# Optimization experiments

Hardware: AMD Instinct MI355X
Metric: run time of the kernel (lower is better)

## Reference

```python
import jax, jax.numpy as jnp
import numpy as np


def setup_inputs() -> dict:
    key = jax.random.key(0)
    ks = jax.random.split(key, 9)
    B, T, C = 4, 2048, 2048
    E, I, SI = 8, 1408, 5632
    s = lambda k, shape, fan_in: jax.random.normal(k, shape, jnp.float32) * (fan_in ** -0.5)
    return {
        "x": jax.random.normal(ks[0], (B, T, C), jnp.float32),
        "gate_w": s(ks[1], (C, E), C),                  # router: x @ gate_w -> [N,E]
        "expert_gate_w": s(ks[2], (E, C, I), C),        # stacked gate_proj weights
        "expert_up_w": s(ks[3], (E, C, I), C),          # stacked up_proj weights
        "expert_down_w": s(ks[4], (E, I, C), I),        # stacked down_proj weights
        "shared_gate_w": s(ks[5], (C, SI), C),
        "shared_up_w": s(ks[6], (C, SI), C),
        "shared_down_w": s(ks[7], (SI, C), SI),
        "shared_expert_gate_w": s(ks[8], (C, 1), C),
        "top_k": 4,
    }


def reference(x, gate_w, expert_gate_w, expert_up_w, expert_down_w,
              shared_gate_w, shared_up_w, shared_down_w, shared_expert_gate_w, top_k):
    B, T, C = x.shape
    E = gate_w.shape[1]
    xf = x.reshape(-1, C)                      # [N, C]
    N = xf.shape[0]

    # --- router: softmax (fp32) -> top-k -> renormalize ---
    logits = xf @ gate_w                       # [N, E]
    probs = jax.nn.softmax(logits.astype(jnp.float32), axis=-1)
    w, idx = jax.lax.top_k(probs, top_k)       # [N, k]
    w = w / jnp.sum(w, axis=-1, keepdims=True)

    # dense combine gates [N, E]: zero for non-selected experts (equivalent to
    # the torch dispatch/sort/combine: each token gets weight w_k on expert idx_k)
    gates = jnp.zeros((N, E), jnp.float32).at[jnp.arange(N)[:, None], idx].add(w)

    # --- per-expert SwiGLU MLP, accumulated via scan over experts ---
    def step(acc, ew):
        wg, wu, wd, g = ew                     # wg/wu: [C,I], wd: [I,C], g: [N]
        h = jax.nn.silu(xf @ wg) * (xf @ wu)   # [N, I]
        return acc + g[:, None] * (h @ wd), None

    routed, _ = jax.lax.scan(
        step, jnp.zeros_like(xf),
        (expert_gate_w, expert_up_w, expert_down_w, gates.T))

    # --- shared expert with sigmoid gate ---
    shared = (jax.nn.silu(xf @ shared_gate_w) * (xf @ shared_up_w)) @ shared_down_w
    sg = jax.nn.sigmoid(xf @ shared_expert_gate_w)   # [N, 1]

    return (routed + sg * shared).reshape(B, T, C)
```

## Files before the change

### kernel.cpp

```cpp
#include <hip/hip_runtime.h>
#include <hip/hip_bf16.h>
#include <stdint.h>


typedef float f32x4 __attribute__((ext_vector_type(4)));
typedef int   i32x4 __attribute__((ext_vector_type(4)));
typedef __hip_bfloat16 bf16;

#define DEV __device__ __forceinline__

DEV void mfma16(f32x4& c, const i32x4& a, const i32x4& b) {
    asm("v_mfma_f32_16x16x32_bf16 %0, %1, %2, %0" : "+v"(c) : "v"(a), "v"(b));
}

template<int ROWS>
DEV void stage(const bf16* gtile, long ldK, char* lds, int tid) {
    const int wid = tid >> 6, lane = tid & 63;
    const int swz = ((lane & 7) ^ (lane >> 3)) << 4;
    constexpr int NISS = (ROWS * 128) / 4096;
    #pragma unroll
    for (int i = 0; i < NISS; i++) {
        const int o = i * 4096 + wid * 1024;
        const int row = (o >> 7) + (lane >> 3);
        const char* ga = (const char*)gtile + (long)row * (ldK * 2) + swz;
        __builtin_amdgcn_global_load_lds(
            (const __attribute__((address_space(1))) void*)ga,
            (__attribute__((address_space(3))) void*)(lds + o), 16, 0, 0);
    }
}

template<int ROWS>
DEV void stage_idx(const char* base, const long* roff, int ktb, char* lds,
                   int tid, int swz) {
    const int wid = tid >> 6;
    constexpr int NISS = (ROWS * 128) / 4096;
    #pragma unroll
    for (int i = 0; i < NISS; i++) {
        const int o = i * 4096 + wid * 1024;
        const char* ga = base + roff[i] + ktb + swz;
        __builtin_amdgcn_global_load_lds(
            (const __attribute__((address_space(1))) void*)ga,
            (__attribute__((address_space(3))) void*)(lds + o), 16, 0, 0);
    }
}

DEV i32x4 ldsfrag(const char* lds, int row, int kbyte) {
    const int off = (row << 7) + (kbyte ^ ((row & 7) << 4));
    return *(const i32x4*)(lds + off);
}

__global__ __launch_bounds__(256) void tcvt(const float* __restrict__ src,
        bf16* __restrict__ dst, int Cd, long dld) {
    __shared__ float t[64][65];
    const int cb = blockIdx.x * 64, rb = blockIdx.y * 64;
    const int tx = threadIdx.x & 63, ty = threadIdx.x >> 6;
    #pragma unroll
    for (int i = 0; i < 16; i++) {
        const int r = ty + i * 4;
        t[r][tx] = src[(long)(rb + r) * Cd + cb + tx];
    }
    __syncthreads();
    #pragma unroll
    for (int i = 0; i < 16; i++) {
        const int c = ty + i * 4;
        dst[(long)(cb + c) * dld + rb + tx] = __float2bfloat16(t[tx][c]);
    }
}

__global__ __launch_bounds__(256) void cvtx(const float* __restrict__ x,
        bf16* __restrict__ xb, long n4) {
    long i = (long)blockIdx.x * blockDim.x + threadIdx.x;
    const long stride = (long)gridDim.x * blockDim.x;
    for (; i < n4; i += stride) {
        const float4 v = ((const float4*)x)[i];
        union { bf16 h[4]; ushort4 u; } cu;
        cu.h[0] = __float2bfloat16(v.x); cu.h[1] = __float2bfloat16(v.y);
        cu.h[2] = __float2bfloat16(v.z); cu.h[3] = __float2bfloat16(v.w);
        ((ushort4*)xb)[i] = cu.u;
    }
}

__global__ __launch_bounds__(256) void router(const float* __restrict__ x,
        const float* __restrict__ gw, const float* __restrict__ segw,
        int* __restrict__ tidx, float* __restrict__ tw,
        float* __restrict__ sg, int C) {
    const int lane = threadIdx.x & 63;
    const long t = (long)blockIdx.x * 4 + (threadIdx.x >> 6);
    const float* xr = x + t * C;
    float a[9];
    #pragma unroll
    for (int e = 0; e < 9; e++) a[e] = 0.f;
    for (int c = lane; c < C; c += 64) {
        const float xv = xr[c];
        const float4* g4 = (const float4*)(gw + (long)c * 8);
        const float4 g0 = g4[0], g1 = g4[1];
        a[0] += xv * g0.x; a[1] += xv * g0.y; a[2] += xv * g0.z; a[3] += xv * g0.w;
        a[4] += xv * g1.x; a[5] += xv * g1.y; a[6] += xv * g1.z; a[7] += xv * g1.w;
        a[8] += xv * segw[c];
    }
    #pragma unroll
    for (int e = 0; e < 9; e++) {
        #pragma unroll
        for (int o = 32; o; o >>= 1) a[e] += __shfl_xor(a[e], o, 64);
    }
    if (lane == 0) {
        float m = a[0];
        #pragma unroll
        for (int e = 1; e < 8; e++) m = fmaxf(m, a[e]);
        float p[8]; float s = 0.f;
        #pragma unroll
        for (int e = 0; e < 8; e++) { p[e] = expf(a[e] - m); s += p[e]; }
        #pragma unroll
        for (int e = 0; e < 8; e++) p[e] /= s;
        bool used[8] = {false,false,false,false,false,false,false,false};
        float wsum = 0.f; int idx[4]; float wv[4];
        for (int k = 0; k < 4; k++) {
            float best = -1.f; int bi = 0;
            for (int e = 0; e < 8; e++)
                if (!used[e] && p[e] > best) { best = p[e]; bi = e; }
            used[bi] = true; idx[k] = bi; wv[k] = best; wsum += best;
        }
        int4 iv; float4 wv4;
        iv.x = idx[0]; iv.y = idx[1]; iv.z = idx[2]; iv.w = idx[3];
        wv4.x = wv[0] / wsum; wv4.y = wv[1] / wsum;
        wv4.z = wv[2] / wsum; wv4.w = wv[3] / wsum;
        ((int4*)tidx)[t] = iv;
        ((float4*)tw)[t] = wv4;
        sg[t] = 1.f / (1.f + expf(-a[8]));
    }
}

__global__ __launch_bounds__(256) void build_lists(const int* __restrict__ tidx,
        const float* __restrict__ tw, int* __restrict__ tok,
        float* __restrict__ wl, int* __restrict__ cnt, int N) {
    const int e = blockIdx.x;
    const int tid = threadIdx.x;
    const int per = N / 256;
    __shared__ int csum[256];
    int c = 0;
    for (int i = 0; i < per; i++) {
        const int4 id4 = ((const int4*)tidx)[tid * per + i];
        if (id4.x == e || id4.y == e || id4.z == e || id4.w == e) c++;
    }
    csum[tid] = c;
    __syncthreads();
    for (int o = 1; o < 256; o <<= 1) {
        const int v = (tid >= o) ? csum[tid - o] : 0;
        __syncthreads();
        csum[tid] += v;
        __syncthreads();
    }
    int pos = csum[tid] - c;
    if (tid == 255) cnt[e] = csum[255];
    for (int i = 0; i < per; i++) {
        const int t = tid * per + i;
        const int4   id4 = ((const int4*)tidx)[t];
        const float4 w4  = ((const float4*)tw)[t];
        float w = 0.f; int hit = 0;
        if      (id4.x == e) { w = w4.x; hit = 1; }
        else if (id4.y == e) { w = w4.y; hit = 1; }
        else if (id4.z == e) { w = w4.z; hit = 1; }
        else if (id4.w == e) { w = w4.w; hit = 1; }
        if (hit) { tok[(long)e * N + pos] = t; wl[(long)e * N + pos] = w; pos++; }
    }
}

__global__ __launch_bounds__(256) void dual_gemm(const bf16* __restrict__ A,
        const int* __restrict__ ridx, const int* __restrict__ cntp, int Mfix,
        const bf16* __restrict__ BG, const bf16* __restrict__ BU,
        bf16* __restrict__ H, long hld,
        const float* __restrict__ sc, int K) {
    __shared__ __align__(128) char Al[16384];
    __shared__ __align__(128) char Gl[8192];
    __shared__ __align__(128) char Ul[8192];
    const int Me = cntp ? *cntp : Mfix;
    const long m0 = (long)blockIdx.x * 128;
    if (m0 >= Me) return;
    const int tid = threadIdx.x, lane = tid & 63, wid = tid >> 6;
    const long n0 = (long)blockIdx.y * 64;
    const int wm = (wid >> 1) * 64, wn = (wid & 1) * 32;
    const int l15 = lane & 15, lhi = lane >> 4;
    const int swz = ((lane & 7) ^ (lane >> 3)) << 4;
    long roffA[4];
    #pragma unroll
    for (int i = 0; i < 4; i++) {
        const int rit = ((i * 4096 + wid * 1024) >> 7) + (lane >> 3);
        int g = (int)m0 + rit;
        if (ridx) g = ridx[g < Me ? g : Me - 1];
        roffA[i] = (long)g * (K * 2);
    }
    f32x4 ag[4][2] = {}; f32x4 au[4][2] = {};
    for (int kt = 0; kt < K; kt += 64) {
        stage_idx<128>((const char*)A, roffA, kt * 2, Al, tid, swz);
        stage<64>(BG + n0 * K + kt, (long)K, Gl, tid);
        stage<64>(BU + n0 * K + kt, (long)K, Ul, tid);
        __syncthreads();
        #pragma unroll
        for (int ks = 0; ks < 2; ks++) {
            const int kb = ks * 64 + lhi * 16;
            i32x4 af[4], bg[2], bu[2];
            #pragma unroll
            for (int mi = 0; mi < 4; mi++) af[mi] = ldsfrag(Al, wm + mi * 16 + l15, kb);
            #pragma unroll
            for (int ni = 0; ni < 2; ni++) {
                bg[ni] = ldsfrag(Gl, wn + ni * 16 + l15, kb);
                bu[ni] = ldsfrag(Ul, wn + ni * 16 + l15, kb);
            }
            #pragma unroll
            for (int mi = 0; mi < 4; mi++) {
                #pragma unroll
                for (int ni = 0; ni < 2; ni++) {
                    mfma16(ag[mi][ni], af[mi], bg[ni]);
                    mfma16(au[mi][ni], af[mi], bu[ni]);
                }
            }
        }
        __syncthreads();
    }
    asm volatile("s_nop 7\n\ts_nop 7\n\ts_nop 7");
    #pragma unroll
    for (int mi = 0; mi < 4; mi++) {
        #pragma unroll
        for (int r = 0; r < 4; r++) {
            const int pos = (int)m0 + wm + mi * 16 + lhi * 4 + r;
            if (pos < Me) {
                const float s = sc[pos];
                #pragma unroll
                for (int ni = 0; ni < 2; ni++) {
                    const float gv = ag[mi][ni][r], uv = au[mi][ni][r];
                    const float h = (gv / (1.f + expf(-gv))) * uv * s;
                    H[(long)pos * hld + n0 + wn + ni * 16 + l15] = __float2bfloat16(h);
                }
            }
        }
    }
}

__global__ __launch_bounds__(256) void gemm_down(const bf16* __restrict__ A,
        const bf16* __restrict__ BT, float* __restrict__ C,
        const int* __restrict__ ridx, const int* __restrict__ cntp, int Mfix,
        int K, long ldc, int beta) {
    __shared__ __align__(128) char Al[16384];
    __shared__ __align__(128) char Bl[16384];
    const int Me = cntp ? *cntp : Mfix;
    const long m0 = (long)blockIdx.y * 128;
    if (m0 >= Me) return;
    const int tid = threadIdx.x, lane = tid & 63, wid = tid >> 6;
    const long n0 = (long)blockIdx.x * 128;
    const int wm = (wid >> 1) * 64, wn = (wid & 1) * 64;
    const int l15 = lane & 15, lhi = lane >> 4;
    f32x4 acc[4][4] = {};
    for (int kt = 0; kt < K; kt += 64) {
        stage<128>(A  + m0 * K + kt, (long)K, Al, tid);
        stage<128>(BT + n0 * K + kt, (long)K, Bl, tid);
        __syncthreads();
        #pragma unroll
        for (int ks = 0; ks < 2; ks++) {
            const int kb = ks * 64 + lhi * 16;
            i32x4 af[4], bfr[4];
            #pragma unroll
            for (int mi = 0; mi < 4; mi++) af[mi]  = ldsfrag(Al, wm + mi * 16 + l15, kb);
            #pragma unroll
            for (int ni = 0; ni < 4; ni++) bfr[ni] = ldsfrag(Bl, wn + ni * 16 + l15, kb);
            #pragma unroll
            for (int mi = 0; mi < 4; mi++) {
                #pragma unroll
                for (int ni = 0; ni < 4; ni++) mfma16(acc[mi][ni], af[mi], bfr[ni]);
            }
        }
        __syncthreads();
    }
    asm volatile("s_nop 7\n\ts_nop 7\n\ts_nop 7");
    #pragma unroll
    for (int mi = 0; mi < 4; mi++) {
        #pragma unroll
        for (int r = 0; r < 4; r++) {
            const int pos = (int)m0 + wm + mi * 16 + lhi * 4 + r;
            if (pos < Me) {
                const long orow = ridx ? (long)ridx[pos] : (long)pos;
                #pragma unroll
                for (int ni = 0; ni < 4; ni++) {
                    const long ci = orow * ldc + n0 + wn + ni * 16 + l15;
                    float v = acc[mi][ni][r];
                    if (beta) v += C[ci];
                    C[ci] = v;
                }
            }
        }
    }
}

extern "C" void kernel_launch(void* const* d_in, const int* in_sizes, int n_in,
                              void* d_out, int out_size, void* d_ws, size_t ws_size,
                              hipStream_t stream) {
    const int N = 8192, Cdim = 2048, E = 8, I = 1408, SI = 5632;

    const float* x    = (const float*)d_in[0];
    const float* gw   = (const float*)d_in[1];
    const float* egw  = (const float*)d_in[2];
    const float* euw  = (const float*)d_in[3];
    const float* edw  = (const float*)d_in[4];
    const float* sgw  = (const float*)d_in[5];
    const float* suw  = (const float*)d_in[6];
    const float* sdw  = (const float*)d_in[7];
    const float* segw = (const float*)d_in[8];
    float* out = (float*)d_out;

    char* ws = (char*)d_ws;
    size_t off = 0;
    auto alloc = [&](size_t bytes) { char* p = ws + off; off += (bytes + 255) & ~(size_t)255; return p; };

    bf16*  xb   = (bf16*) alloc((size_t)N * Cdim * 2);
    int*   tidx = (int*)  alloc((size_t)N * 4 * 4);
    float* tw   = (float*)alloc((size_t)N * 4 * 4);
    float* sg   = (float*)alloc((size_t)N * 4);
    int*   tok  = (int*)  alloc((size_t)E * N * 4);
    float* wl   = (float*)alloc((size_t)E * N * 4);
    int*   cnt  = (int*)  alloc(256);
    const size_t commonEnd = off;

    bf16* Wu   = (bf16*)alloc((size_t)I * Cdim * 2);
    bf16* WgWd = (bf16*)alloc((size_t)I * Cdim * 2);
    bf16* Hc   = (bf16*)alloc((size_t)N * I * 2);
    if (off > ws_size) return;

    cvtx<<<4096, 256, 0, stream>>>(x, xb, (long)N * Cdim / 4);
    router<<<N / 4, 256, 0, stream>>>(x, gw, segw, tidx, tw, sg, Cdim);
    build_lists<<<E, 256, 0, stream>>>(tidx, tw, tok, wl, cnt, N);

    const size_t bigSharedNeed = commonEnd
        + 2 * (size_t)SI * Cdim * 2 + (size_t)N * SI * 2 + 4096;
    if (ws_size >= bigSharedNeed) {
        size_t qoff = commonEnd;
        auto qalloc = [&](size_t bytes) { char* p = ws + qoff; qoff += (bytes + 255) & ~(size_t)255; return p; };
        bf16* WgsWds = (bf16*)qalloc((size_t)SI * Cdim * 2);
        bf16* Wus    = (bf16*)qalloc((size_t)SI * Cdim * 2);
        bf16* Hcs    = (bf16*)qalloc((size_t)N * SI * 2);
        tcvt<<<dim3(SI / 64, Cdim / 64), 256, 0, stream>>>(sgw, WgsWds, SI, (long)Cdim);
        tcvt<<<dim3(SI / 64, Cdim / 64), 256, 0, stream>>>(suw, Wus,    SI, (long)Cdim);
        dual_gemm<<<dim3(N / 128, SI / 64), 256, 0, stream>>>(xb, nullptr, nullptr, N,
                WgsWds, Wus, Hcs, (long)SI, sg, Cdim);
        tcvt<<<dim3(Cdim / 64, SI / 64), 256, 0, stream>>>(sdw, WgsWds, Cdim, (long)SI);
        gemm_down<<<dim3(Cdim / 128, N / 128), 256, 0, stream>>>(Hcs, WgsWds, out,
                nullptr, nullptr, N, SI, (long)Cdim, 0);
    } else {
        for (int s = 0; s < SI / I; s++) {
            const long col0 = (long)s * I;
            tcvt<<<dim3(I / 64, Cdim / 64), 256, 0, stream>>>(sgw + col0, WgWd, SI, (long)Cdim);
            tcvt<<<dim3(I / 64, Cdim / 64), 256, 0, stream>>>(suw + col0, Wu,   SI, (long)Cdim);
            dual_gemm<<<dim3(N / 128, I / 64), 256, 0, stream>>>(xb, nullptr, nullptr, N,
                    WgWd, Wu, Hc, (long)I, sg, Cdim);
            tcvt<<<dim3(Cdim / 64, I / 64), 256, 0, stream>>>(sdw + col0 * Cdim, WgWd, Cdim, (long)I);
            gemm_down<<<dim3(Cdim / 128, N / 128), 256, 0, stream>>>(Hc, WgWd, out,
                    nullptr, nullptr, N, I, (long)Cdim, s > 0);
        }
    }

    for (int e = 0; e < E; e++) {
        const float* gsrc = egw + (long)e * Cdim * I;
        const float* usrc = euw + (long)e * Cdim * I;
        const float* dsrc = edw + (long)e * I * Cdim;
        tcvt<<<dim3(I / 64, Cdim / 64), 256, 0, stream>>>(gsrc, WgWd, I, (long)Cdim);
        tcvt<<<dim3(I / 64, Cdim / 64), 256, 0, stream>>>(usrc, Wu,   I, (long)Cdim);
        dual_gemm<<<dim3(N / 128, I / 64), 256, 0, stream>>>(xb, tok + (long)e * N,
                cnt + e, 0, WgWd, Wu, Hc, (long)I, wl + (long)e * N, Cdim);
        tcvt<<<dim3(Cdim / 64, I / 64), 256, 0, stream>>>(dsrc, WgWd, Cdim, (long)I);
        gemm_down<<<dim3(Cdim / 128, N / 128), 256, 0, stream>>>(Hc, WgWd, out,
                tok + (long)e * N, cnt + e, 0, I, (long)Cdim, 1);
    }
}
```

Measured before the change: 1.724 ms.

## Batch four experts per launch for weight conversion and gate/up GEMM

```diff
diff --git a/kernel.cpp b/kernel.cpp
--- a/kernel.cpp
+++ b/kernel.cpp
@@ -50,8 +50,10 @@
 }
 
 __global__ __launch_bounds__(256) void tcvt(const float* __restrict__ src,
-        bf16* __restrict__ dst, int Cd, long dld) {
+        bf16* __restrict__ dst, int Cd, long dld, long sz, long dz) {
     __shared__ float t[64][65];
+    const long z = blockIdx.z;
+    src += z * sz; dst += z * dz;
     const int cb = blockIdx.x * 64, rb = blockIdx.y * 64;
     const int tx = threadIdx.x & 63, ty = threadIdx.x >> 6;
     #pragma unroll
@@ -166,16 +168,23 @@
 }
 
 __global__ __launch_bounds__(256) void dual_gemm(const bf16* __restrict__ A,
-        const int* __restrict__ ridx, const int* __restrict__ cntp, int Mfix,
-        const bf16* __restrict__ BG, const bf16* __restrict__ BU,
-        bf16* __restrict__ H, long hld,
-        const float* __restrict__ sc, int K) {
+        const int* __restrict__ tok, long tokz,
+        const int* __restrict__ cnt, int Mfix,
+        const bf16* __restrict__ BG0, const bf16* __restrict__ BU0, long bz,
+        bf16* __restrict__ H0, long hld, long hz,
+        const float* __restrict__ sc0, long scz, int K) {
     __shared__ __align__(128) char Al[16384];
     __shared__ __align__(128) char Gl[8192];
     __shared__ __align__(128) char Ul[8192];
-    const int Me = cntp ? *cntp : Mfix;
+    const int z = blockIdx.z;
+    const int Me = cnt ? cnt[z] : Mfix;
     const long m0 = (long)blockIdx.x * 128;
     if (m0 >= Me) return;
+    const int* ridx = tok ? tok + (long)z * tokz : nullptr;
+    const bf16* BG = BG0 + (long)z * bz;
+    const bf16* BU = BU0 + (long)z * bz;
+    bf16* H = H0 + (long)z * hz;
+    const float* sc = sc0 + (long)z * scz;
     const int tid = threadIdx.x, lane = tid & 63, wid = tid >> 6;
     const long n0 = (long)blockIdx.y * 64;
     const int wm = (wid >> 1) * 64, wn = (wid & 1) * 32;
@@ -317,55 +326,47 @@
     int*   tok  = (int*)  alloc((size_t)E * N * 4);
     float* wl   = (float*)alloc((size_t)E * N * 4);
     int*   cnt  = (int*)  alloc(256);
-    const size_t commonEnd = off;
-
-    bf16* Wu   = (bf16*)alloc((size_t)I * Cdim * 2);
-    bf16* WgWd = (bf16*)alloc((size_t)I * Cdim * 2);
-    bf16* Hc   = (bf16*)alloc((size_t)N * I * 2);
+
+    const size_t WSLOT = (size_t)SI * Cdim * 2;
+    bf16* Wa = (bf16*)alloc(WSLOT);
+    bf16* Wb = (bf16*)alloc(WSLOT);
+    bf16* Wc = (bf16*)alloc(WSLOT);
+    bf16* Hc = (bf16*)alloc((size_t)N * SI * 2);
     if (off > ws_size) return;
 
     cvtx<<<4096, 256, 0, stream>>>(x, xb, (long)N * Cdim / 4);
     router<<<N / 4, 256, 0, stream>>>(x, gw, segw, tidx, tw, sg, Cdim);
     build_lists<<<E, 256, 0, stream>>>(tidx, tw, tok, wl, cnt, N);
 
-    const size_t bigSharedNeed = commonEnd
-        + 2 * (size_t)SI * Cdim * 2 + (size_t)N * SI * 2 + 4096;
-    if (ws_size >= bigSharedNeed) {
-        size_t qoff = commonEnd;
-        auto qalloc = [&](size_t bytes) { char* p = ws + qoff; qoff += (bytes + 255) & ~(size_t)255; return p; };
-        bf16* WgsWds = (bf16*)qalloc((size_t)SI * Cdim * 2);
-        bf16* Wus    = (bf16*)qalloc((size_t)SI * Cdim * 2);
-        bf16* Hcs    = (bf16*)qalloc((size_t)N * SI * 2);
-        tcvt<<<dim3(SI / 64, Cdim / 64), 256, 0, stream>>>(sgw, WgsWds, SI, (long)Cdim);
-        tcvt<<<dim3(SI / 64, Cdim / 64), 256, 0, stream>>>(suw, Wus,    SI, (long)Cdim);
-        dual_gemm<<<dim3(N / 128, SI / 64), 256, 0, stream>>>(xb, nullptr, nullptr, N,
-                WgsWds, Wus, Hcs, (long)SI, sg, Cdim);
-        tcvt<<<dim3(Cdim / 64, SI / 64), 256, 0, stream>>>(sdw, WgsWds, Cdim, (long)SI);
-        gemm_down<<<dim3(Cdim / 128, N / 128), 256, 0, stream>>>(Hcs, WgsWds, out,
-                nullptr, nullptr, N, SI, (long)Cdim, 0);
-    } else {
-        for (int s = 0; s < SI / I; s++) {
-            const long col0 = (long)s * I;
-            tcvt<<<dim3(I / 64, Cdim / 64), 256, 0, stream>>>(sgw + col0, WgWd, SI, (long)Cdim);
-            tcvt<<<dim3(I / 64, Cdim / 64), 256, 0, stream>>>(suw + col0, Wu,   SI, (long)Cdim);
-            dual_gemm<<<dim3(N / 128, I / 64), 256, 0, stream>>>(xb, nullptr, nullptr, N,
-                    WgWd, Wu, Hc, (long)I, sg, Cdim);
-            tcvt<<<dim3(Cdim / 64, I / 64), 256, 0, stream>>>(sdw + col0 * Cdim, WgWd, Cdim, (long)I);
-            gemm_down<<<dim3(Cdim / 128, N / 128), 256, 0, stream>>>(Hc, WgWd, out,
-                    nullptr, nullptr, N, I, (long)Cdim, s > 0);
-        }
-    }
-
-    for (int e = 0; e < E; e++) {
-        const float* gsrc = egw + (long)e * Cdim * I;
-        const float* usrc = euw + (long)e * Cdim * I;
-        const float* dsrc = edw + (long)e * I * Cdim;
-        tcvt<<<dim3(I / 64, Cdim / 64), 256, 0, stream>>>(gsrc, WgWd, I, (long)Cdim);
-        tcvt<<<dim3(I / 64, Cdim / 64), 256, 0, stream>>>(usrc, Wu,   I, (long)Cdim);
-        dual_gemm<<<dim3(N / 128, I / 64), 256, 0, stream>>>(xb, tok + (long)e * N,
-                cnt + e, 0, WgWd, Wu, Hc, (long)I, wl + (long)e * N, Cdim);
-        tcvt<<<dim3(Cdim / 64, I / 64), 256, 0, stream>>>(dsrc, WgWd, Cdim, (long)I);
-        gemm_down<<<dim3(Cdim / 128, N / 128), 256, 0, stream>>>(Hc, WgWd, out,
-                tok + (long)e * N, cnt + e, 0, I, (long)Cdim, 1);
-    }
-}
+    tcvt<<<dim3(SI / 64, Cdim / 64, 1), 256, 0, stream>>>(sgw, Wa, SI, (long)Cdim, 0, 0);
+    tcvt<<<dim3(SI / 64, Cdim / 64, 1), 256, 0, stream>>>(suw, Wb, SI, (long)Cdim, 0, 0);
+    tcvt<<<dim3(Cdim / 64, SI / 64, 1), 256, 0, stream>>>(sdw, Wc, Cdim, (long)SI, 0, 0);
+    dual_gemm<<<dim3(N / 128, SI / 64, 1), 256, 0, stream>>>(xb,
+            nullptr, 0, nullptr, N, Wa, Wb, 0, Hc, (long)SI, 0, sg, 0, Cdim);
+    gemm_down<<<dim3(Cdim / 128, N / 128), 256, 0, stream>>>(Hc, Wc, out,
+            nullptr, nullptr, N, SI, (long)Cdim, 0);
+
+    for (int b = 0; b < 2; b++) {
+        const int e0 = b * 4;
+        tcvt<<<dim3(I / 64, Cdim / 64, 4), 256, 0, stream>>>(
+                egw + (long)e0 * Cdim * I, Wa, I, (long)Cdim,
+                (long)Cdim * I, (long)I * Cdim);
+        tcvt<<<dim3(I / 64, Cdim / 64, 4), 256, 0, stream>>>(
+                euw + (long)e0 * Cdim * I, Wb, I, (long)Cdim,
+                (long)Cdim * I, (long)I * Cdim);
+        tcvt<<<dim3(Cdim / 64, I / 64, 4), 256, 0, stream>>>(
+                edw + (long)e0 * I * Cdim, Wc, Cdim, (long)I,
+                (long)I * Cdim, (long)Cdim * I);
+        dual_gemm<<<dim3(N / 128, I / 64, 4), 256, 0, stream>>>(xb,
+                tok + (long)e0 * N, (long)N, cnt + e0, 0,
+                Wa, Wb, (long)I * Cdim,
+                Hc, (long)I, (long)N * I,
+                wl + (long)e0 * N, (long)N, Cdim);
+        for (int z = 0; z < 4; z++) {
+            gemm_down<<<dim3(Cdim / 128, N / 128), 256, 0, stream>>>(
+                    Hc + (long)z * N * I, Wc + (long)z * Cdim * I, out,
+                    tok + (long)(e0 + z) * N, cnt + e0 + z, 0,
+                    I, (long)Cdim, 1);
+        }
+    }
+}
```

Result: faster. 1.642 ms (-4.8%).
